# Performance work log

Measured on AMD Instinct MI355X. Metric: run time of the kernel, lower is better.

Reference implementation:

```python
import jax, jax.numpy as jnp
import numpy as np

VOCAB, E = 50000, 256          # embedding table
WH, SH = 256, 256              # word_hidden_size, sent_hidden_size
DM = WH // 2                   # d_model of both S4Models = 128
NC = (WH // 2) // 2            # complex state modes N//2 = 64
FACTOR = 2
LN_EPS = 1e-5


def _s4model(x, encW, encb, log_dt, Cre, Cim, logAre, Aim, D,
             convW, convb, lng, lnb, d1W, d1b, d2W, d2b, pooling):
    """S4Model forward (eval mode, n_layers=1). x: (B, L, d_input)."""
    x = x @ encW + encb                      # (B, L, H)
    u = jnp.swapaxes(x, -1, -2)              # (B, H, L)
    L = u.shape[-1]
    # --- S4D kernel (Vandermonde) ---
    dt = jnp.exp(log_dt)                     # (H,)
    C = Cre + 1j * Cim                       # (H, N)
    A = -jnp.exp(logAre) + 1j * Aim          # (H, N)
    dtA = A * dt[:, None]                    # (H, N)
    K = jnp.exp(dtA[:, :, None] * jnp.arange(L))           # (H, N, L)
    Ck = C * (jnp.exp(dtA) - 1.0) / A
    k = 2.0 * jnp.einsum('hn,hnl->hl', Ck, K).real         # (H, L)
    # --- FFT convolution ---
    kf = jnp.fft.rfft(k, n=2 * L)            # (H, L+1)
    uf = jnp.fft.rfft(u, n=2 * L)            # (B, H, L+1)
    y = jnp.fft.irfft(uf * kf, n=2 * L)[..., :L]
    y = y + u * D[:, None]
    y = jax.nn.gelu(y, approximate=False)
    # 1x1 conv to 2H then GLU over channel dim
    y = jnp.einsum('oh,bhl->bol', convW, y) + convb[:, None]
    a, b = jnp.split(y, 2, axis=-2)
    z = a * jax.nn.sigmoid(b)
    x = z + u                                # residual
    xt = jnp.swapaxes(x, -1, -2)             # (B, L, H)
    mu = jnp.mean(xt, axis=-1, keepdims=True)
    var = jnp.var(xt, axis=-1, keepdims=True)
    xt = (xt - mu) / jnp.sqrt(var + LN_EPS) * lng + lnb
    h = jax.nn.gelu(xt @ d1W + d1b, approximate=False)
    out = h @ d2W + d2b                      # (B, L, d_output)
    return out.mean(axis=1) if pooling else out


def _model_params(key, d_input, d_model, n, d_output, factor):
    ks = jax.random.split(key, 16)
    H, N = d_model, n
    import math
    p = {}
    p['encW'] = jax.random.normal(ks[0], (d_input, H)) * 0.02
    p['encb'] = jnp.zeros((H,))
    p['log_dt'] = jax.random.uniform(ks[1], (H,)) * (math.log(0.1) - math.log(0.001)) + math.log(0.001)
    p['Cre'] = jax.random.normal(ks[2], (H, N))
    p['Cim'] = jax.random.normal(ks[3], (H, N))
    p['logAre'] = jnp.log(0.5 * jnp.ones((H, N)))
    p['Aim'] = math.pi * jnp.broadcast_to(jnp.arange(N, dtype=jnp.float32), (H, N))
    p['D'] = jax.random.normal(ks[4], (H,))
    p['convW'] = jax.random.normal(ks[5], (2 * H, H)) * 0.05
    p['convb'] = jnp.zeros((2 * H,))
    p['lng'] = jnp.ones((H,))
    p['lnb'] = jnp.zeros((H,))
    p['d1W'] = jax.random.normal(ks[6], (H, H * factor)) * 0.02
    p['d1b'] = jnp.zeros((H * factor,))
    p['d2W'] = jax.random.normal(ks[7], (H * factor, d_output)) * 0.02
    p['d2b'] = jnp.zeros((d_output,))
    return p


def setup_inputs() -> dict:
    key = jax.random.key(0)
    k_ids, k_emb, k_w, k_s = jax.random.split(key, 4)
    inp = {
        'ids': jax.random.randint(k_ids, (8, 64, 512), 0, VOCAB, dtype=jnp.int32),
        'emb': jax.random.normal(k_emb, (VOCAB, E)) * 0.1,
    }
    for pref, k, din, dout in (('w_', k_w, WH, SH), ('s_', k_s, SH, SH)):
        for name, v in _model_params(k, din, DM, NC, dout, FACTOR).items():
            inp[pref + name] = v
    return inp


PNAMES = ['encW', 'encb', 'log_dt', 'Cre', 'Cim', 'logAre', 'Aim', 'D',
          'convW', 'convb', 'lng', 'lnb', 'd1W', 'd1b', 'd2W', 'd2b']


def reference(ids, emb,
              w_encW, w_encb, w_log_dt, w_Cre, w_Cim, w_logAre, w_Aim, w_D,
              w_convW, w_convb, w_lng, w_lnb, w_d1W, w_d1b, w_d2W, w_d2b,
              s_encW, s_encb, s_log_dt, s_Cre, s_Cim, s_logAre, s_Aim, s_D,
              s_convW, s_convb, s_lng, s_lnb, s_d1W, s_d1b, s_d2W, s_d2b):
    B, S, W = ids.shape
    x = emb[ids.reshape(B * S, W)]                       # (B*S, W, E)
    wp = (w_encW, w_encb, w_log_dt, w_Cre, w_Cim, w_logAre, w_Aim, w_D,
          w_convW, w_convb, w_lng, w_lnb, w_d1W, w_d1b, w_d2W, w_d2b)
    sents = _s4model(x, *wp, pooling=True)               # (B*S, SH)
    sents = sents.reshape(B, S, SH)
    sp = (s_encW, s_encb, s_log_dt, s_Cre, s_Cim, s_logAre, s_Aim, s_D,
          s_convW, s_convb, s_lng, s_lnb, s_d1W, s_d1b, s_d2W, s_d2b)
    out = _s4model(sents, *sp, pooling=False)            # (B, S, SH)
    return out  # Euclidean manifold: no clipping / expmap0
```

## Files before the change

kernel.cpp:

```cpp
#include <hip/hip_runtime.h>
#include <hip/hip_bf16.h>

#define DEVINL __device__ __forceinline__

typedef _Float16 f16;
typedef _Float16 f16x2 __attribute__((ext_vector_type(2)));
typedef _Float16 f16x8 __attribute__((ext_vector_type(8)));
typedef float f32x4 __attribute__((ext_vector_type(4)));

#define MFMA16 __builtin_amdgcn_mfma_f32_16x16x32_f16

DEVINL float gelu_f(float x) {
    return 0.5f * x * (1.0f + erff(x * 0.70710678118654752440f));
}

DEVINL int swz(int col, int row) {
    return (((col >> 3) ^ (row & 7)) << 3) | (col & 7);
}

__global__ __launch_bounds__(256)
void s4k2_kernel(float* __restrict__ kout,
                 const float* __restrict__ log_dt, const float* __restrict__ Cre,
                 const float* __restrict__ Cim, const float* __restrict__ logAre,
                 const float* __restrict__ Aim, int L)
{
    __shared__ double EaR[64][16], EaI[64][16];
    __shared__ double EbR[64][32], EbI[64][32];
    __shared__ double CkR[64], CkI[64];
    int h = blockIdx.x, tid = threadIdx.x;
    if (tid < 64) {
        int n = tid;
        double dt = exp((double)log_dt[h]);
        double Ar = -exp((double)logAre[h * 64 + n]);
        double Ai = (double)Aim[h * 64 + n];
        double dr = Ar * dt, di = Ai * dt;
        double edr = exp(dr);
        double E1r = edr * cos(di), E1i = edr * sin(di);
        double den = Ar * Ar + Ai * Ai;
        double tr = ((E1r - 1.0) * Ar + E1i * Ai) / den;
        double ti = (E1i * Ar - (E1r - 1.0) * Ai) / den;
        double Cr = (double)Cre[h * 64 + n], Ci = (double)Cim[h * 64 + n];
        CkR[n] = Cr * tr - Ci * ti;
        CkI[n] = Cr * ti + Ci * tr;
        double br = 1.0, bi = 0.0;
        for (int b2 = 0; b2 < 32; ++b2) {
            EbR[n][b2] = br; EbI[n][b2] = bi;
            double nr = br * E1r - bi * E1i;
            bi = br * E1i + bi * E1r; br = nr;
        }
        double E32r = br, E32i = bi;
        double ar2 = 1.0, ai2 = 0.0;
        for (int a = 0; a < 16; ++a) {
            EaR[n][a] = ar2; EaI[n][a] = ai2;
            double nr = ar2 * E32r - ai2 * E32i;
            ai2 = ar2 * E32i + ai2 * E32r; ar2 = nr;
        }
    }
    __syncthreads();
    for (int l = tid; l < L; l += 256) {
        int a = l >> 5, b2 = l & 31;
        double acc = 0.0;
        for (int n = 0; n < 64; ++n) {
            double er = EaR[n][a] * EbR[n][b2] - EaI[n][a] * EbI[n][b2];
            double ei = EaR[n][a] * EbI[n][b2] + EaI[n][a] * EbR[n][b2];
            acc += CkR[n] * er - CkI[n] * ei;
        }
        kout[h * L + l] = (float)(2.0 * acc);
    }
}

__global__ __launch_bounds__(256)
void packemb_kernel(f16* __restrict__ dst, const float* __restrict__ src)
{
    long i = ((long)blockIdx.x * 256 + threadIdx.x) * 8;
    float4 a = *(const float4*)(src + i);
    float4 b = *(const float4*)(src + i + 4);
    f16x8 o;
    o[0]=(f16)a.x; o[1]=(f16)a.y; o[2]=(f16)a.z; o[3]=(f16)a.w;
    o[4]=(f16)b.x; o[5]=(f16)b.y; o[6]=(f16)b.z; o[7]=(f16)b.w;
    *(f16x8*)(dst + i) = o;
}

__global__ __launch_bounds__(256)
void packfrag_kernel(f16* __restrict__ dst, const float* __restrict__ src,
                     int NN, int sk, int so)
{
    int idx = blockIdx.x * 256 + threadIdx.x;
    int e = idx & 7, lane = (idx >> 3) & 63;
    int rem = idx >> 9;
    int nn = rem % NN, kk = rem / NN;
    int o = nn * 16 + (lane & 15);
    int k = kk * 32 + 8 * (lane >> 4) + e;
    dst[idx] = (f16)src[k * sk + o * so];
}

__global__ __launch_bounds__(256)
void toep_kernel(f16* __restrict__ tf, const float* __restrict__ kW)
{
    int idx = blockIdx.x * 256 + threadIdx.x;
    int r = idx & 7;
    int lane = (idx >> 3) & 63;
    int nn = (idx >> 9) & 3;
    int s = (idx >> 11) & 1;
    int d = (idx >> 12) & 7;
    int h = idx >> 15;
    int widx = 64 * d + 16 * nn + (lane & 15) - 32 * s - 8 * (lane >> 4) - r;
    float v = (widx >= 0 && widx < 512) ? kW[h * 512 + widx] : 0.f;
    tf[idx] = (f16)v;
}

__global__ __launch_bounds__(256)
void enc_mfma(const f16* __restrict__ emb16, const int* __restrict__ ids,
              long tok_base, const f16* __restrict__ Wfrag,
              const float* __restrict__ bias, f16* __restrict__ u)
{
    __shared__ f16 zs[128][72];
    int tid = threadIdx.x, wave = tid >> 6, lane = tid & 63;
    long m0 = (long)blockIdx.x * 64;
    int b_local = (int)(m0 >> 9), l0 = (int)(m0 & 511);

    int gidx = ids[tok_base + m0 + 16 * wave + (lane & 15)];
    const f16* arow = emb16 + (long)gidx * 256 + 8 * (lane >> 4);
    const f16* bfp = Wfrag + lane * 8;

    f32x4 acc[8] = {};
#pragma unroll
    for (int kk = 0; kk < 8; ++kk) {
        f16x8 af = *(const f16x8*)(arow + kk * 32);
#pragma unroll
        for (int nn = 0; nn < 8; ++nn) {
            f16x8 bf = *(const f16x8*)(bfp + (kk * 8 + nn) * 512);
            acc[nn] = MFMA16(af, bf, acc[nn], 0, 0, 0);
        }
    }
#pragma unroll
    for (int nn = 0; nn < 8; ++nn) {
        int h = nn * 16 + (lane & 15);
        float bv = bias[h];
#pragma unroll
        for (int reg = 0; reg < 4; ++reg) {
            int l = 16 * wave + 4 * (lane >> 4) + reg;
            zs[h][l] = (f16)(acc[nn][reg] + bv);
        }
    }
    __syncthreads();
    f16* ub = u + (long)b_local * 65536 + l0;
#pragma unroll
    for (int it = 0; it < 4; ++it) {
        int h = (tid >> 3) + 32 * it, seg = tid & 7;
        *(f16x8*)(ub + (long)h * 512 + seg * 8) = *(const f16x8*)&zs[h][seg * 8];
    }
}

__global__ __launch_bounds__(256)
void conv_mfma(const f16* __restrict__ u, const f16* __restrict__ tf,
               const float* __restrict__ Dv, f16* __restrict__ y, int SC)
{
    __shared__ f16 As[64][72];
    __shared__ f16 ys[64][72];
    int Lt = blockIdx.x, b0 = blockIdx.y * 64, h = blockIdx.z;
    int l0 = Lt * 64;
    int tid = threadIdx.x, wave = tid >> 6, lane = tid & 63;

    f32x4 acc[4] = {};

    int ar = tid >> 2, aseg = tid & 3;
    bool arow_ok = (b0 + ar) < SC;
    const f16* ubase = u + ((long)(b0 + ar) * 128 + h) * 512;

    for (int jt = 0; jt <= Lt; ++jt) {
        f16x8 av0 = {}, av1 = {};
        if (arow_ok) {
            av0 = *(const f16x8*)(ubase + jt * 64 + aseg * 16);
            av1 = *(const f16x8*)(ubase + jt * 64 + aseg * 16 + 8);
        }
        __syncthreads();
        *(f16x8*)&As[ar][aseg * 16]     = av0;
        *(f16x8*)&As[ar][aseg * 16 + 8] = av1;
        __syncthreads();
        int d = Lt - jt;
        const f16* tfb = tf + (((long)h * 8 + d) * 8) * 512 + lane * 8;
#pragma unroll 2
        for (int s = 0; s < 2; ++s) {
            f16x8 af = *(const f16x8*)&As[16 * wave + (lane & 15)][32 * s + 8 * (lane >> 4)];
#pragma unroll
            for (int nn = 0; nn < 4; ++nn) {
                f16x8 bf = *(const f16x8*)(tfb + ((long)s * 4 + nn) * 512);
                acc[nn] = MFMA16(af, bf, acc[nn], 0, 0, 0);
            }
        }
    }
    float Dh = Dv[h];
#pragma unroll
    for (int nn = 0; nn < 4; ++nn) {
#pragma unroll
        for (int reg = 0; reg < 4; ++reg) {
            int bl = 16 * wave + 4 * (lane >> 4) + reg;
            int ll = 16 * nn + (lane & 15);
            ys[bl][ll] = (f16)gelu_f(acc[nn][reg] + (float)As[bl][ll] * Dh);
        }
    }
    __syncthreads();
#pragma unroll
    for (int it = 0; it < 2; ++it) {
        int unit = tid + 256 * it;
        int r = unit >> 3, seg = unit & 7;
        if (b0 + r < SC)
            *(f16x8*)(y + ((long)(b0 + r) * 128 + h) * 512 + l0 + seg * 8)
                = *(const f16x8*)&ys[r][seg * 8];
    }
}

#define PITCH 144
__global__ __launch_bounds__(256)
void glu_mfma(const f16* __restrict__ y, const f16* __restrict__ u,
              const f16* __restrict__ Wfrag, const float* __restrict__ cb,
              const float* __restrict__ lng, const float* __restrict__ lnb,
              f16* __restrict__ xt)
{
    __shared__ f16 At[64][PITCH];
    __shared__ f16 Ut[64][PITCH];
    int b = blockIdx.x, l0 = blockIdx.y * 64;
    int tid = threadIdx.x, wave = tid >> 6, lane = tid & 63;

#pragma unroll
    for (int it = 0; it < 2; ++it) {
        int unit = tid + 256 * it;
        int hp = unit & 63, seg = unit >> 6;
        int h = hp * 2;
        const f16* yp = y + ((long)b * 128 + h) * 512 + l0 + seg * 8;
        const f16* up = u + ((long)b * 128 + h) * 512 + l0 + seg * 8;
        f16x8 ya = *(const f16x8*)yp;
        f16x8 yb = *(const f16x8*)(yp + 512);
        f16x8 ua = *(const f16x8*)up;
        f16x8 ub = *(const f16x8*)(up + 512);
#pragma unroll
        for (int q = 0; q < 8; ++q) {
            int l = seg * 8 + q;
            int ix = swz(h, l);
            f16x2 py; py[0] = ya[q]; py[1] = yb[q];
            f16x2 pu; pu[0] = ua[q]; pu[1] = ub[q];
            *(f16x2*)&At[l][ix] = py;
            *(f16x2*)&Ut[l][ix] = pu;
        }
    }
    __syncthreads();

    f32x4 acc[16] = {};
    const f16* bfp = Wfrag + lane * 8;
    int arow = 16 * wave + (lane & 15);
#pragma unroll
    for (int kk = 0; kk < 4; ++kk) {
        f16x8 af = *(const f16x8*)&At[arow][swz(kk * 32 + 8 * (lane >> 4), arow)];
#pragma unroll
        for (int nn = 0; nn < 16; ++nn) {
            f16x8 bf = *(const f16x8*)(bfp + (kk * 16 + nn) * 512);
            acc[nn] = MFMA16(af, bf, acc[nn], 0, 0, 0);
        }
    }

    float zz[8][4];
    float sum[4] = {0.f,0.f,0.f,0.f}, sq[4] = {0.f,0.f,0.f,0.f};
#pragma unroll
    for (int nn = 0; nn < 8; ++nn) {
        int o = nn * 16 + (lane & 15);
        float ca = cb[o], cbb = cb[o + 128];
#pragma unroll
        for (int reg = 0; reg < 4; ++reg) {
            int l = 16 * wave + 4 * (lane >> 4) + reg;
            float a = acc[nn][reg] + ca;
            float bbv = acc[nn + 8][reg] + cbb;
            float z = a * (1.0f / (1.0f + expf(-bbv))) + (float)Ut[l][swz(o, l)];
            zz[nn][reg] = z;
            sum[reg] += z; sq[reg] += z * z;
        }
    }
#pragma unroll
    for (int d = 1; d < 16; d <<= 1) {
#pragma unroll
        for (int reg = 0; reg < 4; ++reg) {
            sum[reg] += __shfl_xor(sum[reg], d);
            sq[reg]  += __shfl_xor(sq[reg], d);
        }
    }
    float mu[4], rs[4];
#pragma unroll
    for (int reg = 0; reg < 4; ++reg) {
        mu[reg] = sum[reg] * (1.0f / 128.0f);
        float var = sq[reg] * (1.0f / 128.0f) - mu[reg] * mu[reg];
        rs[reg] = rsqrtf(var + 1e-5f);
    }
#pragma unroll
    for (int nn = 0; nn < 8; ++nn) {
        int o = nn * 16 + (lane & 15);
        float g = lng[o], bta = lnb[o];
#pragma unroll
        for (int reg = 0; reg < 4; ++reg) {
            int l = 16 * wave + 4 * (lane >> 4) + reg;
            At[l][swz(o, l)] = (f16)((zz[nn][reg] - mu[reg]) * rs[reg] * g + bta);
        }
    }
    __syncthreads();
    f16* xb = xt + ((long)b * 512 + l0) * 128;
#pragma unroll
    for (int it = 0; it < 4; ++it) {
        int unit = tid + 256 * it;
        int l = unit >> 4, seg = unit & 15;
        *(f16x8*)(xb + (long)l * 128 + seg * 8)
            = *(const f16x8*)&At[l][(seg ^ (l & 7)) * 8];
    }
}

__global__ __launch_bounds__(256)
void d1_mfma(const f16* __restrict__ xt, const f16* __restrict__ Wfrag,
             const float* __restrict__ b1, float* __restrict__ hbar,
             long tok_base)
{
    __shared__ float red[4][16][16];
    int tid = threadIdx.x, wave = tid >> 6, lane = tid & 63;
    long m0 = (long)blockIdx.x * 64;

    const f16* arow = xt + (m0 + 16 * wave + (lane & 15)) * 128 + 8 * (lane >> 4);
    const f16* bfp = Wfrag + lane * 8;

    f32x4 acc[16] = {};
#pragma unroll
    for (int kk = 0; kk < 4; ++kk) {
        f16x8 af = *(const f16x8*)(arow + kk * 32);
#pragma unroll
        for (int nn = 0; nn < 16; ++nn) {
            f16x8 bf = *(const f16x8*)(bfp + (kk * 16 + nn) * 512);
            acc[nn] = MFMA16(af, bf, acc[nn], 0, 0, 0);
        }
    }
    long sent = (tok_base + m0) >> 9;
#pragma unroll
    for (int nn = 0; nn < 16; ++nn) {
        float bv = b1[nn * 16 + (lane & 15)];
        float s = 0.f;
#pragma unroll
        for (int reg = 0; reg < 4; ++reg)
            s += gelu_f(acc[nn][reg] + bv);
        s += __shfl_xor(s, 16);
        s += __shfl_xor(s, 32);
        if (lane < 16) red[wave][lane][nn] = s;
    }
    __syncthreads();
    if (wave == 0 && lane < 16) {
#pragma unroll
        for (int nn = 0; nn < 16; ++nn) {
            float tot = red[0][lane][nn] + red[1][lane][nn]
                      + red[2][lane][nn] + red[3][lane][nn];
            atomicAdd(&hbar[sent * 256 + nn * 16 + lane], tot * (1.0f / 512.0f));
        }
    }
}

__global__ __launch_bounds__(256)
void gemm_kernel(const float* __restrict__ A, const int* __restrict__ gather,
                 const float* __restrict__ W, const float* __restrict__ bias,
                 float* __restrict__ C, float* __restrict__ pool,
                 long m_base, int K, int N, int act, int poolLen)
{
    __shared__ float As[32][68];
    __shared__ float Ws[32][128];
    __shared__ float red[16][128];

    int tid = threadIdx.x;
    int tx = tid & 15, ty = tid >> 4;
    long m0 = (long)blockIdx.x * 64;
    int n0 = blockIdx.y * 128;

    int la_row = tid >> 2, la_k = (tid & 3) * 8;
    long arow = gather ? (long)gather[m_base + m0 + la_row] : (m0 + la_row);
    const float* Arow = A + arow * (long)K + la_k;
    int wk = tid >> 3, wn = (tid & 7) * 16;
    const float* Wp = W + (long)wk * N + n0 + wn;

    float acc[4][8];
#pragma unroll
    for (int i = 0; i < 4; ++i)
#pragma unroll
        for (int j = 0; j < 8; ++j) acc[i][j] = 0.f;

    for (int k0 = 0; k0 < K; k0 += 32) {
        float4 a0 = *(const float4*)(Arow + k0);
        float4 a1 = *(const float4*)(Arow + k0 + 4);
        const float* wp = Wp + (long)k0 * N;
        float4 w0 = *(const float4*)(wp);
        float4 w1 = *(const float4*)(wp + 4);
        float4 w2 = *(const float4*)(wp + 8);
        float4 w3 = *(const float4*)(wp + 12);
        __syncthreads();
        As[la_k + 0][la_row] = a0.x; As[la_k + 1][la_row] = a0.y;
        As[la_k + 2][la_row] = a0.z; As[la_k + 3][la_row] = a0.w;
        As[la_k + 4][la_row] = a1.x; As[la_k + 5][la_row] = a1.y;
        As[la_k + 6][la_row] = a1.z; As[la_k + 7][la_row] = a1.w;
        *(float4*)&Ws[wk][wn]      = w0;
        *(float4*)&Ws[wk][wn + 4]  = w1;
        *(float4*)&Ws[wk][wn + 8]  = w2;
        *(float4*)&Ws[wk][wn + 12] = w3;
        __syncthreads();
#pragma unroll
        for (int kk = 0; kk < 32; ++kk) {
            float4 av  = *(const float4*)&As[kk][ty * 4];
            float4 wv0 = *(const float4*)&Ws[kk][tx * 4];
            float4 wv1 = *(const float4*)&Ws[kk][64 + tx * 4];
            float a_[4] = {av.x, av.y, av.z, av.w};
            float w_[8] = {wv0.x, wv0.y, wv0.z, wv0.w, wv1.x, wv1.y, wv1.z, wv1.w};
#pragma unroll
            for (int i = 0; i < 4; ++i)
#pragma unroll
                for (int j = 0; j < 8; ++j)
                    acc[i][j] = fmaf(a_[i], w_[j], acc[i][j]);
        }
    }

    float bv[8];
#pragma unroll
    for (int j = 0; j < 8; ++j) {
        int col = (j < 4) ? (tx * 4 + j) : (64 + tx * 4 + (j - 4));
        bv[j] = bias[n0 + col];
    }
#pragma unroll
    for (int i = 0; i < 4; ++i)
#pragma unroll
        for (int j = 0; j < 8; ++j) {
            float v = acc[i][j] + bv[j];
            if (act == 1) v = gelu_f(v);
            acc[i][j] = v;
        }

    if (pool) {
        float pv[8];
#pragma unroll
        for (int j = 0; j < 8; ++j)
            pv[j] = acc[0][j] + acc[1][j] + acc[2][j] + acc[3][j];
        __syncthreads();
#pragma unroll
        for (int j = 0; j < 8; ++j) {
            int col = (j < 4) ? (tx * 4 + j) : (64 + tx * 4 + (j - 4));
            red[ty][col] = pv[j];
        }
        __syncthreads();
        if (ty == 0) {
            long sent = (m_base + m0) / poolLen;
            float inv = 1.0f / (float)poolLen;
#pragma unroll
            for (int j = 0; j < 8; ++j) {
                int col = (j < 4) ? (tx * 4 + j) : (64 + tx * 4 + (j - 4));
                float s = 0.f;
#pragma unroll
                for (int t = 0; t < 16; ++t) s += red[t][col];
                atomicAdd(&pool[sent * N + n0 + col], s * inv);
            }
        }
    } else if (C) {
#pragma unroll
        for (int i = 0; i < 4; ++i) {
            long m = m0 + ty * 4 + i;
            float* cp = C + m * (long)N + n0;
            float4 s0 = {acc[i][0], acc[i][1], acc[i][2], acc[i][3]};
            float4 s1 = {acc[i][4], acc[i][5], acc[i][6], acc[i][7]};
            *(float4*)(cp + tx * 4) = s0;
            *(float4*)(cp + 64 + tx * 4) = s1;
        }
    }
}

__global__ __launch_bounds__(256)
void transpose_kernel(const float* __restrict__ in, float* __restrict__ out,
                      int L, int H)
{
    __shared__ float t[32][33];
    int b = blockIdx.x, l0 = blockIdx.y * 32, h0 = blockIdx.z * 32;
    int tid = threadIdx.x;
    int c = tid & 31, r = tid >> 5;
    const float* ib = in + ((long)b * L + l0) * H + h0;
#pragma unroll
    for (int i = 0; i < 4; ++i)
        t[r + 8 * i][c] = ib[(long)(r + 8 * i) * H + c];
    __syncthreads();
    float* ob = out + ((long)b * H + h0) * L + l0;
#pragma unroll
    for (int i = 0; i < 4; ++i)
        ob[(long)(r + 8 * i) * L + c] = t[c][r + 8 * i];
}

__global__ __launch_bounds__(256)
void conv_kernel(const float* __restrict__ u, const float* __restrict__ kmat,
                 float* __restrict__ y, int NB, int L)
{
    __shared__ float Ut[64][68];
    __shared__ float kwin[128];
    int h = blockIdx.x;
    int b0 = blockIdx.y * 64, l0 = blockIdx.z * 64;
    int tid = threadIdx.x, tx = tid & 15, ty = tid >> 4;
    const float* kh = kmat + (long)h * L;

    float acc[4][4];
#pragma unroll
    for (int i = 0; i < 4; ++i)
#pragma unroll
        for (int j = 0; j < 4; ++j) acc[i][j] = 0.f;

    int ur = tid >> 2, uc = (tid & 3) * 16;

    for (int j0 = 0; j0 <= l0 + 63; j0 += 64) {
        float4 u0 = {0,0,0,0}, u1 = {0,0,0,0}, u2 = {0,0,0,0}, u3 = {0,0,0,0};
        if (b0 + ur < NB) {
            const float* up = u + ((long)(b0 + ur) * 128 + h) * L + j0 + uc;
            u0 = *(const float4*)up;        u1 = *(const float4*)(up + 4);
            u2 = *(const float4*)(up + 8);  u3 = *(const float4*)(up + 12);
        }
        float kv_ = 0.f;
        int d = l0 - j0 - 63 + tid;
        if (tid < 128) kv_ = (d >= 0 && d < L) ? kh[d] : 0.f;
        __syncthreads();
        {
            float uv[16] = {u0.x,u0.y,u0.z,u0.w, u1.x,u1.y,u1.z,u1.w,
                            u2.x,u2.y,u2.z,u2.w, u3.x,u3.y,u3.z,u3.w};
#pragma unroll
            for (int q = 0; q < 16; ++q) Ut[uc + q][ur] = uv[q];
        }
        if (tid < 128) kwin[tid] = kv_;
        __syncthreads();
#pragma unroll
        for (int jj = 0; jj < 64; ++jj) {
            float4 uv = *(const float4*)&Ut[jj][ty * 4];
            float ub[4] = {uv.x, uv.y, uv.z, uv.w};
            float kj[4];
#pragma unroll
            for (int j = 0; j < 4; ++j) kj[j] = kwin[63 + tx * 4 + j - jj];
#pragma unroll
            for (int i = 0; i < 4; ++i)
#pragma unroll
                for (int j = 0; j < 4; ++j)
                    acc[i][j] = fmaf(ub[i], kj[j], acc[i][j]);
        }
    }
#pragma unroll
    for (int i = 0; i < 4; ++i) {
        int b = b0 + ty * 4 + i;
        if (b < NB) {
            float4 s = {acc[i][0], acc[i][1], acc[i][2], acc[i][3]};
            *(float4*)(y + ((long)b * 128 + h) * L + l0 + tx * 4) = s;
        }
    }
}

__global__ __launch_bounds__(256)
void skipgelu_kernel(float* __restrict__ y, const float* __restrict__ u,
                     const float* __restrict__ D, int log2L, long total)
{
    long i = (long)blockIdx.x * 256 + threadIdx.x;
    long stride = (long)gridDim.x * 256;
    for (; i < total; i += stride) {
        int h = (int)((i >> log2L) & 127);
        float v = y[i] + u[i] * D[h];
        y[i] = gelu_f(v);
    }
}

__global__ __launch_bounds__(256)
void glu_kernel(const float* __restrict__ convW, const float* __restrict__ convb,
                const float* __restrict__ g, const float* u,
                float* z, int L)
{
    __shared__ float Wa[32][68], Wb[32][68], Gs[32][72];
    int b = blockIdx.x, o0 = blockIdx.y * 64, l0 = blockIdx.z * 64;
    int tid = threadIdx.x, tx = tid & 15, ty = tid >> 4;
    const float* gb = g + (long)b * 128 * L;

    float aa[4][4], ab[4][4];
#pragma unroll
    for (int i = 0; i < 4; ++i)
#pragma unroll
        for (int j = 0; j < 4; ++j) { aa[i][j] = 0.f; ab[i][j] = 0.f; }

    int wr = tid >> 2, wc = (tid & 3) * 8;
    int gh = tid >> 3, gl = (tid & 7) * 8;

    for (int k0 = 0; k0 < 128; k0 += 32) {
        float4 wa0 = *(const float4*)(convW + (long)(o0 + wr) * 128 + k0 + wc);
        float4 wa1 = *(const float4*)(convW + (long)(o0 + wr) * 128 + k0 + wc + 4);
        float4 wb0 = *(const float4*)(convW + (long)(o0 + wr + 128) * 128 + k0 + wc);
        float4 wb1 = *(const float4*)(convW + (long)(o0 + wr + 128) * 128 + k0 + wc + 4);
        float4 g0 = *(const float4*)(gb + (long)(k0 + gh) * L + l0 + gl);
        float4 g1 = *(const float4*)(gb + (long)(k0 + gh) * L + l0 + gl + 4);
        __syncthreads();
        {
            float wav[8] = {wa0.x,wa0.y,wa0.z,wa0.w, wa1.x,wa1.y,wa1.z,wa1.w};
            float wbv[8] = {wb0.x,wb0.y,wb0.z,wb0.w, wb1.x,wb1.y,wb1.z,wb1.w};
#pragma unroll
            for (int q = 0; q < 8; ++q) { Wa[wc + q][wr] = wav[q]; Wb[wc + q][wr] = wbv[q]; }
        }
        *(float4*)&Gs[gh][gl]     = g0;
        *(float4*)&Gs[gh][gl + 4] = g1;
        __syncthreads();
#pragma unroll
        for (int kk = 0; kk < 32; ++kk) {
            float4 wav = *(const float4*)&Wa[kk][ty * 4];
            float4 wbv = *(const float4*)&Wb[kk][ty * 4];
            float4 gv  = *(const float4*)&Gs[kk][tx * 4];
            float wa_[4] = {wav.x, wav.y, wav.z, wav.w};
            float wb_[4] = {wbv.x, wbv.y, wbv.z, wbv.w};
            float g_[4]  = {gv.x, gv.y, gv.z, gv.w};
#pragma unroll
            for (int i = 0; i < 4; ++i)
#pragma unroll
                for (int j = 0; j < 4; ++j) {
                    aa[i][j] = fmaf(wa_[i], g_[j], aa[i][j]);
                    ab[i][j] = fmaf(wb_[i], g_[j], ab[i][j]);
                }
        }
    }
#pragma unroll
    for (int i = 0; i < 4; ++i) {
        int o = o0 + ty * 4 + i;
        float ca = convb[o], cb2 = convb[o + 128];
        const float* up = u + ((long)b * 128 + o) * L + l0 + tx * 4;
        float4 uv = *(const float4*)up;
        float uu[4] = {uv.x, uv.y, uv.z, uv.w};
        float tmp[4];
#pragma unroll
        for (int j = 0; j < 4; ++j) {
            float av = aa[i][j] + ca;
            float bv2 = ab[i][j] + cb2;
            tmp[j] = av * (1.0f / (1.0f + expf(-bv2))) + uu[j];
        }
        float4 outv = {tmp[0], tmp[1], tmp[2], tmp[3]};
        *(float4*)(z + ((long)b * 128 + o) * L + l0 + tx * 4) = outv;
    }
}

__global__ __launch_bounds__(256)
void ln_kernel(const float* __restrict__ z, const float* __restrict__ gamma,
               const float* __restrict__ beta, float* __restrict__ out, int L)
{
    __shared__ float zs[128][65];
    __shared__ float mu_s[64], rs_s[64];
    int b = blockIdx.x, l0 = blockIdx.y * 64;
    const float* zb = z + (long)b * 128 * L;
    int tid = threadIdx.x;
    for (int idx = tid; idx < 128 * 64; idx += 256) {
        int h = idx >> 6, li = idx & 63;
        zs[h][li] = zb[(long)h * L + l0 + li];
    }
    __syncthreads();
    int l = tid >> 2, sub = tid & 3;
    float s = 0.f, sq = 0.f;
    for (int ii = 0; ii < 32; ++ii) {
        int i = (ii + sub * 8) & 31;
        float v = zs[sub * 32 + i][l];
        s += v; sq += v * v;
    }
    s += __shfl_xor(s, 1); sq += __shfl_xor(sq, 1);
    s += __shfl_xor(s, 2); sq += __shfl_xor(sq, 2);
    if (sub == 0) {
        float mu = s * (1.0f / 128.0f);
        float var = sq * (1.0f / 128.0f) - mu * mu;
        mu_s[l] = mu;
        rs_s[l] = rsqrtf(var + 1e-5f);
    }
    __syncthreads();
    for (int idx = tid; idx < 64 * 128; idx += 256) {
        int li = idx >> 7, h = idx & 127;
        float v = (zs[h][li] - mu_s[li]) * rs_s[li];
        out[((long)b * L + l0 + li) * 128 + h] = v * gamma[h] + beta[h];
    }
}

extern "C" void kernel_launch(void* const* d_in, const int* in_sizes, int n_in,
                              void* d_out, int out_size, void* d_ws, size_t ws_size,
                              hipStream_t stream)
{
    const int* ids = (const int*)d_in[0];
    const float* emb = (const float*)d_in[1];
    const float* const* wp = (const float* const*)(d_in + 2);
    const float* const* sp = (const float* const*)(d_in + 18);
    enum {ENCW = 0, ENCB, LOGDT, CRE, CIM, LOGARE, AIM, DD,
          CONVW, CONVB, LNG, LNB, D1W, D1B, D2W, D2B};

    char* p = (char*)d_ws;
    auto alloc = [&](size_t bytes) {
        char* r = p; p += (bytes + 255) & ~(size_t)255; return r;
    };
    float* kW    = (float*)alloc(128 * 512 * 4);
    float* kS    = (float*)alloc(128 * 64 * 4);
    float* sents = (float*)alloc(512 * 256 * 4);
    float* hbar  = (float*)alloc(512 * 256 * 4);
    float* su    = (float*)alloc(512 * 128 * 4);
    float* subhl = (float*)alloc(512 * 128 * 4);
    float* sy    = (float*)alloc(512 * 128 * 4);
    float* szb   = (float*)alloc(512 * 128 * 4);
    float* sxt   = (float*)alloc(512 * 128 * 4);
    float* sh    = (float*)alloc(512 * 256 * 4);
    f16* encF    = (f16*)alloc(32768 * 2);
    f16* convF   = (f16*)alloc(32768 * 2);
    f16* d1F     = (f16*)alloc(32768 * 2);
    f16* tf      = (f16*)alloc(4194304L * 2);
    f16* emb16   = (f16*)alloc(12800000L * 2);

    long avail = (long)ws_size - (long)(p - (char*)d_ws);
    int SC = 512;
    while (SC > 1 && 3L * SC * 65536 * 2 + 1024 > avail) SC >>= 1;
    int nch = 512 / SC;
    f16* u_c  = (f16*)alloc((size_t)SC * 65536 * 2);
    f16* y_c  = (f16*)alloc((size_t)SC * 65536 * 2);
    f16* xt_c = (f16*)alloc((size_t)SC * 65536 * 2);

    hipMemsetAsync(hbar, 0, 512 * 256 * 4, stream);
    packemb_kernel<<<6250, 256, 0, stream>>>(emb16, emb);
    s4k2_kernel<<<128, 256, 0, stream>>>(
        kW, wp[LOGDT], wp[CRE], wp[CIM], wp[LOGARE], wp[AIM], 512);
    s4k2_kernel<<<128, 256, 0, stream>>>(
        kS, sp[LOGDT], sp[CRE], sp[CIM], sp[LOGARE], sp[AIM], 64);
    packfrag_kernel<<<128, 256, 0, stream>>>(encF, wp[ENCW], 8, 128, 1);
    packfrag_kernel<<<128, 256, 0, stream>>>(convF, wp[CONVW], 16, 1, 128);
    packfrag_kernel<<<128, 256, 0, stream>>>(d1F, wp[D1W], 16, 256, 1);
    toep_kernel<<<16384, 256, 0, stream>>>(tf, kW);

    for (int c = 0; c < nch; ++c) {
        long tok_base = (long)c * SC * 512;
        enc_mfma<<<SC * 8, 256, 0, stream>>>(
            emb16, ids, tok_base, encF, wp[ENCB], u_c);
        conv_mfma<<<dim3(8, (SC + 63) / 64, 128), 256, 0, stream>>>(
            u_c, tf, wp[DD], y_c, SC);
        glu_mfma<<<dim3(SC, 8), 256, 0, stream>>>(
            y_c, u_c, convF, wp[CONVB], wp[LNG], wp[LNB], xt_c);
        d1_mfma<<<SC * 8, 256, 0, stream>>>(
            xt_c, d1F, wp[D1B], hbar, tok_base);
    }
    gemm_kernel<<<dim3(8, 2), 256, 0, stream>>>(
        hbar, nullptr, wp[D2W], wp[D2B], sents, nullptr, 0, 256, 256, 0, 0);

    gemm_kernel<<<dim3(8, 1), 256, 0, stream>>>(
        sents, nullptr, sp[ENCW], sp[ENCB], su, nullptr, 0, 256, 128, 0, 0);
    transpose_kernel<<<dim3(8, 2, 4), 256, 0, stream>>>(su, subhl, 64, 128);
    conv_kernel<<<dim3(128, 1, 1), 256, 0, stream>>>(subhl, kS, sy, 8, 64);
    skipgelu_kernel<<<256, 256, 0, stream>>>(sy, subhl, sp[DD], 6, 8L * 128 * 64);
    glu_kernel<<<dim3(8, 2, 1), 256, 0, stream>>>(
        sp[CONVW], sp[CONVB], sy, subhl, szb, 64);
    ln_kernel<<<dim3(8, 1), 256, 0, stream>>>(szb, sp[LNG], sp[LNB], sxt, 64);
    gemm_kernel<<<dim3(8, 2), 256, 0, stream>>>(
        sxt, nullptr, sp[D1W], sp[D1B], sh, nullptr, 0, 128, 256, 1, 0);
    gemm_kernel<<<dim3(8, 2), 256, 0, stream>>>(
        sh, nullptr, sp[D2W], sp[D2B], (float*)d_out, nullptr, 0, 256, 256, 0, 0);
}
```

Measured before the change: 615.2 us.

## Fuse GLU/LayerNorm with d1 GEMM and load conv A-fragments directly from global

The GLU+LayerNorm kernel and the d1 GEMM+GELU+mean-pool kernel become one kernel. The normalized tile stays in LDS and feeds the d1 MFMAs directly, so the xt intermediate is never written to or read back from global memory, and one launch per chunk is dropped. Separately, conv_mfma no longer stages u tiles through LDS with two barriers per iteration. Each lane loads its MFMA A-fragment straight from global memory and re-reads u for the D skip term in the epilogue, trading LDS traffic and syncs for uncoalesced global reads and higher register pressure in the fused kernel.

```diff
diff --git a/kernel.cpp b/kernel.cpp
--- a/kernel.cpp
+++ b/kernel.cpp
@@ -156,33 +156,22 @@
 void conv_mfma(const f16* __restrict__ u, const f16* __restrict__ tf,
                const float* __restrict__ Dv, f16* __restrict__ y, int SC)
 {
-    __shared__ f16 As[64][72];
     __shared__ f16 ys[64][72];
     int Lt = blockIdx.x, b0 = blockIdx.y * 64, h = blockIdx.z;
     int l0 = Lt * 64;
     int tid = threadIdx.x, wave = tid >> 6, lane = tid & 63;
 
     f32x4 acc[4] = {};
-
-    int ar = tid >> 2, aseg = tid & 3;
-    bool arow_ok = (b0 + ar) < SC;
-    const f16* ubase = u + ((long)(b0 + ar) * 128 + h) * 512;
+    int arow = 16 * wave + (lane & 15);
+    bool arow_ok = (b0 + arow) < SC;
+    const f16* abase = u + ((long)(b0 + arow) * 128 + h) * 512 + 8 * (lane >> 4);
 
     for (int jt = 0; jt <= Lt; ++jt) {
-        f16x8 av0 = {}, av1 = {};
-        if (arow_ok) {
-            av0 = *(const f16x8*)(ubase + jt * 64 + aseg * 16);
-            av1 = *(const f16x8*)(ubase + jt * 64 + aseg * 16 + 8);
-        }
-        __syncthreads();
-        *(f16x8*)&As[ar][aseg * 16]     = av0;
-        *(f16x8*)&As[ar][aseg * 16 + 8] = av1;
-        __syncthreads();
-        int d = Lt - jt;
-        const f16* tfb = tf + (((long)h * 8 + d) * 8) * 512 + lane * 8;
-#pragma unroll 2
+        const f16* tfb = tf + (((long)h * 8 + (Lt - jt)) * 8) * 512 + lane * 8;
+#pragma unroll
         for (int s = 0; s < 2; ++s) {
-            f16x8 af = *(const f16x8*)&As[16 * wave + (lane & 15)][32 * s + 8 * (lane >> 4)];
+            f16x8 af = {};
+            if (arow_ok) af = *(const f16x8*)(abase + jt * 64 + 32 * s);
 #pragma unroll
             for (int nn = 0; nn < 4; ++nn) {
                 f16x8 bf = *(const f16x8*)(tfb + ((long)s * 4 + nn) * 512);
@@ -197,7 +186,10 @@
         for (int reg = 0; reg < 4; ++reg) {
             int bl = 16 * wave + 4 * (lane >> 4) + reg;
             int ll = 16 * nn + (lane & 15);
-            ys[bl][ll] = (f16)gelu_f(acc[nn][reg] + (float)As[bl][ll] * Dh);
+            float uv = 0.f;
+            if (b0 + bl < SC)
+                uv = (float)u[((long)(b0 + bl) * 128 + h) * 512 + l0 + ll];
+            ys[bl][ll] = (f16)gelu_f(acc[nn][reg] + uv * Dh);
         }
     }
     __syncthreads();
@@ -213,13 +205,17 @@
 
 #define PITCH 144
 __global__ __launch_bounds__(256)
-void glu_mfma(const f16* __restrict__ y, const f16* __restrict__ u,
-              const f16* __restrict__ Wfrag, const float* __restrict__ cb,
-              const float* __restrict__ lng, const float* __restrict__ lnb,
-              f16* __restrict__ xt)
+void gld2_mfma(const f16* __restrict__ y, const f16* __restrict__ u,
+               const f16* __restrict__ Wfrag ,
+               const float* __restrict__ cb, const float* __restrict__ lng,
+               const float* __restrict__ lnb,
+               const f16* __restrict__ W1frag ,
+               const float* __restrict__ b1, float* __restrict__ hbar,
+               long sent_base)
 {
     __shared__ f16 At[64][PITCH];
     __shared__ f16 Ut[64][PITCH];
+    __shared__ float red[4][16][16];
     int b = blockIdx.x, l0 = blockIdx.y * 64;
     int tid = threadIdx.x, wave = tid >> 6, lane = tid & 63;
 
@@ -301,46 +297,27 @@
         }
     }
     __syncthreads();
-    f16* xb = xt + ((long)b * 512 + l0) * 128;
-#pragma unroll
-    for (int it = 0; it < 4; ++it) {
-        int unit = tid + 256 * it;
-        int l = unit >> 4, seg = unit & 15;
-        *(f16x8*)(xb + (long)l * 128 + seg * 8)
-            = *(const f16x8*)&At[l][(seg ^ (l & 7)) * 8];
-    }
-}
-
-__global__ __launch_bounds__(256)
-void d1_mfma(const f16* __restrict__ xt, const f16* __restrict__ Wfrag,
-             const float* __restrict__ b1, float* __restrict__ hbar,
-             long tok_base)
-{
-    __shared__ float red[4][16][16];
-    int tid = threadIdx.x, wave = tid >> 6, lane = tid & 63;
-    long m0 = (long)blockIdx.x * 64;
-
-    const f16* arow = xt + (m0 + 16 * wave + (lane & 15)) * 128 + 8 * (lane >> 4);
-    const f16* bfp = Wfrag + lane * 8;
-
-    f32x4 acc[16] = {};
+
+    f32x4 acc2[16] = {};
+    const f16* b1fp = W1frag + lane * 8;
 #pragma unroll
     for (int kk = 0; kk < 4; ++kk) {
-        f16x8 af = *(const f16x8*)(arow + kk * 32);
+        f16x8 af = *(const f16x8*)&At[arow][swz(kk * 32 + 8 * (lane >> 4), arow)];
 #pragma unroll
         for (int nn = 0; nn < 16; ++nn) {
-            f16x8 bf = *(const f16x8*)(bfp + (kk * 16 + nn) * 512);
-            acc[nn] = MFMA16(af, bf, acc[nn], 0, 0, 0);
-        }
-    }
-    long sent = (tok_base + m0) >> 9;
+            f16x8 bf = *(const f16x8*)(b1fp + (kk * 16 + nn) * 512);
+            acc2[nn] = MFMA16(af, bf, acc2[nn], 0, 0, 0);
+        }
+    }
+
+    long sent = sent_base + b;
 #pragma unroll
     for (int nn = 0; nn < 16; ++nn) {
         float bv = b1[nn * 16 + (lane & 15)];
         float s = 0.f;
 #pragma unroll
         for (int reg = 0; reg < 4; ++reg)
-            s += gelu_f(acc[nn][reg] + bv);
+            s += gelu_f(acc2[nn][reg] + bv);
         s += __shfl_xor(s, 16);
         s += __shfl_xor(s, 32);
         if (lane < 16) red[wave][lane][nn] = s;
@@ -704,11 +681,10 @@
 
     long avail = (long)ws_size - (long)(p - (char*)d_ws);
     int SC = 512;
-    while (SC > 1 && 3L * SC * 65536 * 2 + 1024 > avail) SC >>= 1;
+    while (SC > 1 && 2L * SC * 131072 + 1024 > avail) SC >>= 1;
     int nch = 512 / SC;
-    f16* u_c  = (f16*)alloc((size_t)SC * 65536 * 2);
-    f16* y_c  = (f16*)alloc((size_t)SC * 65536 * 2);
-    f16* xt_c = (f16*)alloc((size_t)SC * 65536 * 2);
+    f16* u_c = (f16*)alloc((size_t)SC * 65536 * 2);
+    f16* y_c = (f16*)alloc((size_t)SC * 65536 * 2);
 
     hipMemsetAsync(hbar, 0, 512 * 256 * 4, stream);
     packemb_kernel<<<6250, 256, 0, stream>>>(emb16, emb);
@@ -727,10 +703,9 @@
             emb16, ids, tok_base, encF, wp[ENCB], u_c);
         conv_mfma<<<dim3(8, (SC + 63) / 64, 128), 256, 0, stream>>>(
             u_c, tf, wp[DD], y_c, SC);
-        glu_mfma<<<dim3(SC, 8), 256, 0, stream>>>(
-            y_c, u_c, convF, wp[CONVB], wp[LNG], wp[LNB], xt_c);
-        d1_mfma<<<SC * 8, 256, 0, stream>>>(
-            xt_c, d1F, wp[D1B], hbar, tok_base);
+        gld2_mfma<<<dim3(SC, 8), 256, 0, stream>>>(
+            y_c, u_c, convF, wp[CONVB], wp[LNG], wp[LNB],
+            d1F, wp[D1B], hbar, (long)c * SC);
     }
     gemm_kernel<<<dim3(8, 2), 256, 0, stream>>>(
         hbar, nullptr, wp[D2W], wp[D2B], sents, nullptr, 0, 256, 256, 0, 0);
```

After: 642.2 us. 4.4% more time.
